# Performance work log

Hardware: AMD Instinct MI355X
Metric: run time of the kernel (lower is better)

Reference implementation:

```python
import math
import jax, jax.numpy as jnp
import numpy as np
from jax import lax

W_DIM = 512
UP = 2
K = 3
LRELU_GAIN = math.sqrt(2.0)  # bias_act def_gain for 'lrelu'
CLAMP = 256.0                # conv_clamp * gain(=1)


def setup_inputs() -> dict:
    key = jax.random.key(0)
    ks = jax.random.split(key, 8)
    B, Cin, Cout, H = 16, 512, 512, 32
    return {
        "x": jax.random.normal(ks[0], (B, Cin, H, H), jnp.float32),
        "w_latent": jax.random.normal(ks[1], (B, W_DIM), jnp.float32),
        "affine_weight": jax.random.normal(ks[2], (Cin, W_DIM), jnp.float32),
        "affine_bias": jnp.ones((Cin,), jnp.float32),  # bias_init=1
        "conv_weight": jax.random.normal(ks[3], (Cout, Cin, K, K), jnp.float32),
        "noise": jax.random.normal(ks[4], (B, 1, 2 * H, 2 * H), jnp.float32),
        "noise_strength": jax.random.uniform(ks[5], (1,), jnp.float32),
        "bias": jax.random.normal(ks[6], (Cout,), jnp.float32),
    }


def reference(x, w_latent, affine_weight, affine_bias, conv_weight, noise, noise_strength, bias):
    B, Cin, H, W = x.shape
    Cout = conv_weight.shape[0]

    # EqualFullyConnectedLayer (linear act): style = w @ (W * 1/sqrt(in)).T + b
    style = w_latent @ (affine_weight * (1.0 / math.sqrt(W_DIM))).T + affine_bias  # [B, Cin]

    # Modulate + demodulate per-sample weights: [B, Cout, Cin, K, K]
    wmod = conv_weight[None] * style[:, None, :, None, None]
    dcoefs = lax.rsqrt(jnp.sum(wmod * wmod, axis=(2, 3, 4)) + 1e-8)  # [B, Cout]
    wmod = wmod * dcoefs[:, :, None, None, None]

    # Grouped transposed conv (stride=UP), batch-as-groups trick.
    # torch.conv_transpose2d(x, w.transpose, stride=UP) == dilated conv with
    # spatially-flipped modulated weight, lhs_dilation=UP, padding=K-1.
    w_eff = wmod.reshape(B * Cout, Cin, K, K)[:, :, ::-1, ::-1]
    x1 = x.reshape(1, B * Cin, H, W)
    y = lax.conv_general_dilated(
        x1, w_eff, window_strides=(1, 1),
        padding=[(K - 1, K - 1), (K - 1, K - 1)],
        lhs_dilation=(UP, UP), feature_group_count=B,
        dimension_numbers=("NCHW", "OIHW", "NCHW"))  # [1, B*Cout, 2H+1, 2W+1]

    # upfirdn2d: FIR low-pass (1,3,3,1) outer, normalized, gain=up^2, pad (1,1,1,1)
    f1 = jnp.array([1.0, 3.0, 3.0, 1.0], jnp.float32)
    f2 = jnp.outer(f1, f1)
    f2 = f2 / f2.sum() * (UP * UP)
    yc = y.reshape(B * Cout, 1, 2 * H + 1, 2 * W + 1)
    y = lax.conv_general_dilated(
        yc, f2[None, None], window_strides=(1, 1), padding=[(1, 1), (1, 1)],
        dimension_numbers=("NCHW", "OIHW", "NCHW"))
    y = y.reshape(B, Cout, 2 * H, 2 * W)

    # noise injection + fused bias + lrelu(gain=sqrt(2)) + clamp
    y = y + noise * noise_strength[0]
    y = y + bias[None, :, None, None]
    y = jax.nn.leaky_relu(y, negative_slope=0.2) * LRELU_GAIN
    return jnp.clip(y, -CLAMP, CLAMP)
```

## Files before the change

### kernel.cpp

```cpp
#include <hip/hip_runtime.h>
#include <hip/hip_bf16.h>


typedef unsigned short u16;
typedef unsigned int u32;
typedef u16 u16x8 __attribute__((ext_vector_type(8)));
typedef __bf16 bf16x8 __attribute__((ext_vector_type(8)));
typedef float f32x4 __attribute__((ext_vector_type(4)));

#define NB 16

__device__ __forceinline__ float bf2f(u16 v) {
  unsigned int u = ((unsigned int)v) << 16;
  float f;
  __builtin_memcpy(&f, &u, 4);
  return f;
}
__device__ __forceinline__ u16 f2bf(float f) {
  __hip_bfloat16 h = __float2bfloat16(f);
  u16 r;
  __builtin_memcpy(&r, &h, 2);
  return r;
}
__device__ __forceinline__ void async16(u16* lds, const u16* g) {
  __builtin_amdgcn_global_load_lds(
      (const __attribute__((address_space(1))) u32*)g,
      (__attribute__((address_space(3))) u32*)lds, 16, 0, 0);
}

__global__ __launch_bounds__(256) void k_style(const float* __restrict__ wl,
                                               const float* __restrict__ aw,
                                               const float* __restrict__ ab,
                                               float* __restrict__ style) {
  __shared__ float lw[512];
  const int b = blockIdx.y;
  const int c0 = blockIdx.x << 6;
  const int t = threadIdx.x;
  for (int k = t; k < 512; k += 256) lw[k] = wl[b * 512 + k];
  __syncthreads();
  const int w = t >> 6, l = t & 63;
  const float4 lv0 = *(const float4*)(lw + (l << 2));
  const float4 lv1 = *(const float4*)(lw + 256 + (l << 2));
  for (int r = w; r < 64; r += 4) {
    const int c = c0 + r;
    const float* row = aw + (size_t)c * 512 + (l << 2);
    const float4 a0 = *(const float4*)(row);
    const float4 a1 = *(const float4*)(row + 256);
    float acc = lv0.x * a0.x + lv0.y * a0.y + lv0.z * a0.z + lv0.w * a0.w +
                lv1.x * a1.x + lv1.y * a1.y + lv1.z * a1.z + lv1.w * a1.w;
#pragma unroll
    for (int off = 32; off; off >>= 1) acc += __shfl_down(acc, off, 64);
    if (l == 0) style[b * 512 + c] = acc * 0.04419417382415922f + ab[c];
  }
}

__global__ __launch_bounds__(256) void k_wprep(const float* __restrict__ cw,
                                               const float* __restrict__ style,
                                               float* __restrict__ dcoef,
                                               u16* __restrict__ W2) {
  __shared__ u16 lw[4608];
  __shared__ float wsq[512];
  const int o = blockIdx.x, t = threadIdx.x;
  const float* src = cw + (size_t)o * 4608;
  for (int v = t; v < 4608; v += 256) {
    unsigned c = (unsigned)v / 9u;
    unsigned kp = (unsigned)v % 9u;
    lw[kp * 512 + c] = f2bf(src[v]);
  }
  for (int c = t; c < 512; c += 256) {
    const float* p = src + (size_t)c * 9;
    float s = 0.f;
#pragma unroll
    for (int k = 0; k < 9; ++k) {
      float v = p[k];
      s += v * v;
    }
    wsq[c] = s;
  }
  __syncthreads();
  u16* dst = W2 + (size_t)o * 4608;
  for (int v = t; v < 576; v += 256)
    *(u16x8*)(dst + v * 8) = *(const u16x8*)(lw + v * 8);
  const int w = t >> 6, l = t & 63;
  for (int b = w; b < NB; b += 4) {
    float part = 0.f;
#pragma unroll
    for (int c = l; c < 512; c += 64) {
      float st = style[b * 512 + c];
      part += st * st * wsq[c];
    }
#pragma unroll
    for (int off = 32; off; off >>= 1) part += __shfl_down(part, off, 64);
    if (l == 0) dcoef[b * 512 + o] = 1.0f / sqrtf(part + 1e-8f);
  }
}

__global__ __launch_bounds__(256) void k_xt(const float* __restrict__ x,
                                            const float* __restrict__ style,
                                            u16* __restrict__ xT) {
  __shared__ u16 tile[64 * 66];
  const int b = blockIdx.z, c0 = blockIdx.y << 6, s0 = blockIdx.x << 6;
  const int t = threadIdx.x;
#pragma unroll
  for (int i = 0; i < 16; ++i) {
    int e = i * 256 + t;
    int cc = e >> 6, ss = e & 63;
    int c = c0 + cc;
    float v = x[(size_t)(b * 512 + c) * 1024 + s0 + ss] * style[b * 512 + c];
    tile[cc * 66 + ss] = f2bf(v);
  }
  __syncthreads();
#pragma unroll
  for (int e = 0; e < 2; ++e) {
    int idx = e * 256 + t;
    int sc = idx >> 3;
    int cg = (idx & 7) << 3;
    u16x8 v;
#pragma unroll
    for (int g = 0; g < 8; ++g) v[g] = tile[(cg + g) * 66 + sc];
    *(u16x8*)(xT + (size_t)(b * 1024 + s0 + sc) * 512 + c0 + cg) = v;
  }
}

__global__ __launch_bounds__(512, 2) void k_gemm(const u16* __restrict__ W2,
                                                 const u16* __restrict__ xT,
                                                 u16* __restrict__ Z) {
  __shared__ u16 At[4][8192];
  __shared__ u16 Bt[4][8192];
  const int t = threadIdx.x;
  const int lin = blockIdx.y * 64 + blockIdx.x;
  const int xlog = ((lin & 7) << 3) | ((lin >> 3) & 7);
  const int ylog = lin >> 6;
  const int m0 = ylog << 8;
  const int n0 = xlog << 8;
  const int l = t & 63;
  const int w = t >> 6;
  const int wm = w >> 2;
  const int wn = w & 3;
  const int lrow = l & 15;
  const int lk = l >> 4;

  const int sr = t >> 2;
  const int sch = ((t & 3) + (sr >> 1)) & 3;
  const u16* gA = W2 + (size_t)(m0 + sr) * 512 + (sch << 3);
  const u16* gB = xT + (size_t)(n0 + sr) * 512 + (sch << 3);
  const int wb = w << 9;

  const int sk8 = ((lk - (lrow >> 1)) & 3) << 3;
  const int arow = (wm << 7) + lrow;
  const int brow = (wn << 6) + lrow;

  f32x4 acc[8][4] = {};

#define STAGE_A(nb_, kt_)                                   \
  async16(&At[nb_][wb], gA + (kt_) * 32);                   \
  async16(&At[nb_][4096 + wb], gA + (kt_) * 32 + 65536)
#define STAGE_B(nb_, kt_)                                   \
  async16(&Bt[nb_][wb], gB + (kt_) * 32);                   \
  async16(&Bt[nb_][4096 + wb], gB + (kt_) * 32 + 65536)

  STAGE_A(0, 0);
  STAGE_B(0, 0);
  STAGE_A(1, 1);
  STAGE_B(1, 1);
  STAGE_A(2, 2);
  STAGE_B(2, 2);
  asm volatile("s_waitcnt vmcnt(8)" ::: "memory");
  asm volatile("s_barrier" ::: "memory");

  for (int kt = 0; kt < 16; ++kt) {
    const int buf = kt & 3;
    const int nb = (kt + 3) & 3;
    const u16* Ab = At[buf];
    const u16* Bb = Bt[buf];
    bf16x8 av[4], bv[4], av2[4];

#pragma unroll
    for (int i = 0; i < 4; ++i)
      av[i] = *(const bf16x8*)(Ab + (arow + i * 16) * 32 + sk8);
#pragma unroll
    for (int j = 0; j < 4; ++j)
      bv[j] = *(const bf16x8*)(Bb + (brow + j * 16) * 32 + sk8);
    if (kt < 13) { STAGE_A(nb, kt + 3); }
    asm volatile("s_barrier" ::: "memory");
    asm volatile("s_waitcnt lgkmcnt(0)" ::: "memory");
    __builtin_amdgcn_sched_barrier(0);
    __builtin_amdgcn_s_setprio(1);
#pragma unroll
    for (int i = 0; i < 4; ++i)
#pragma unroll
      for (int j = 0; j < 4; ++j)
        acc[i][j] = __builtin_amdgcn_mfma_f32_16x16x32_bf16(av[i], bv[j], acc[i][j], 0, 0, 0);
    __builtin_amdgcn_s_setprio(0);
    asm volatile("s_barrier" ::: "memory");

#pragma unroll
    for (int i = 0; i < 4; ++i)
      av2[i] = *(const bf16x8*)(Ab + (arow + 64 + i * 16) * 32 + sk8);
    if (kt < 13) { STAGE_B(nb, kt + 3); }
    asm volatile("s_barrier" ::: "memory");
    asm volatile("s_waitcnt lgkmcnt(0)" ::: "memory");
    __builtin_amdgcn_sched_barrier(0);
    __builtin_amdgcn_s_setprio(1);
#pragma unroll
    for (int i = 0; i < 4; ++i)
#pragma unroll
      for (int j = 0; j < 4; ++j)
        acc[i + 4][j] = __builtin_amdgcn_mfma_f32_16x16x32_bf16(av2[i], bv[j], acc[i + 4][j], 0, 0, 0);
    __builtin_amdgcn_s_setprio(0);

    if (kt <= 12) {
      asm volatile("s_waitcnt vmcnt(8)" ::: "memory");
      asm volatile("s_barrier" ::: "memory");
    } else if (kt == 13) {
      asm volatile("s_waitcnt vmcnt(4)" ::: "memory");
      asm volatile("s_barrier" ::: "memory");
    } else if (kt == 14) {
      asm volatile("s_waitcnt vmcnt(0)" ::: "memory");
      asm volatile("s_barrier" ::: "memory");
    }
  }
#undef STAGE_A
#undef STAGE_B

  const int mr = m0 + (wm << 7) + (lk << 2);
  const int nc = n0 + (wn << 6) + lrow;
#pragma unroll
  for (int i = 0; i < 8; ++i)
#pragma unroll
    for (int j = 0; j < 4; ++j)
#pragma unroll
      for (int r = 0; r < 4; ++r)
        Z[(size_t)(mr + i * 16 + r) * 16384 + nc + j * 16] = f2bf(acc[i][j][r]);
}

__global__ __launch_bounds__(256) void k_scatter(
    const u16* __restrict__ Z, const float* __restrict__ dcoef,
    const float* __restrict__ noise, const float* __restrict__ nstr,
    const float* __restrict__ bias, float* __restrict__ out) {
  __shared__ u16 Zl[9 * 1024];
  __shared__ float Hl[3 * 2048];
  const int o = blockIdx.x;
  const int b = blockIdx.y;
  const int t = threadIdx.x;
  const u16* Zp = Z + (size_t)o * 9 * 16384 + (size_t)b * 1024;
  for (int v = t; v < 1152; v += 256) {
    int kp = v >> 7, off = (v & 127) << 3;
    *(u16x8*)(Zl + kp * 1024 + off) = *(const u16x8*)(Zp + (size_t)kp * 16384 + off);
  }
  __syncthreads();
#pragma unroll
  for (int e = 0; e < 12; ++e) {
    int idx = e * 256 + t;
    int ky = idx >> 10;
    int i = (idx >> 5) & 31;
    int j = idx & 31;
    const u16* P0 = Zl + (ky * 3 + 0) * 1024 + i * 32;
    const u16* P1 = P0 + 1024;
    const u16* P2 = P0 + 2048;
    float Ej = bf2f(P0[j]) + (j >= 1 ? bf2f(P2[j - 1]) : 0.f);
    float Ej1 = (j < 31 ? bf2f(P0[j + 1]) : 0.f) + bf2f(P2[j]);
    float Ojm = j >= 1 ? bf2f(P1[j - 1]) : 0.f;
    float Oj = bf2f(P1[j]);
    float Ojp = j < 31 ? bf2f(P1[j + 1]) : 0.f;
    float* hp = Hl + ky * 2048 + i * 64 + j;
    hp[0] = Ojm + 3.f * Ej + 3.f * Oj + Ej1;
    hp[32] = Ej + 3.f * Oj + 3.f * Ej1 + Ojp;
  }
  __syncthreads();
  const float dc = dcoef[b * 512 + o] * 0.0625f;
  const float ns = nstr[0];
  const float bo = bias[o];
  const int n = t & 63;
  const int i0 = (t >> 6) << 3;
  const int sw = ((n & 1) << 5) | (n >> 1);
  const float* H0 = Hl + sw;
  const float* H1 = Hl + 2048 + sw;
  const float* H2 = Hl + 4096 + sw;
  float h0 = H0[i0 * 64];
  float h1 = H1[i0 * 64];
  float h1p = (i0 > 0) ? H1[(i0 - 1) * 64] : 0.f;
  float h2p = (i0 > 0) ? H2[(i0 - 1) * 64] : 0.f;
  const float* nz = noise + ((size_t)b << 12) + n;
  float* op = out + (((size_t)(b * 512 + o)) << 12) + n;
#pragma unroll
  for (int s = 0; s < 8; ++s) {
    int i = i0 + s;
    float h0n = (i < 31) ? H0[(i + 1) * 64] : 0.f;
    float h1n = (i < 31) ? H1[(i + 1) * 64] : 0.f;
    float h2 = H2[i * 64];
    float ev = h1p + 3.f * (h0 + h2p) + 3.f * h1 + (h0n + h2);
    float od = (h0 + h2p) + 3.f * h1 + 3.f * (h0n + h2) + h1n;
    int m = 2 * i;
    float v0 = ev * dc + nz[(size_t)m * 64] * ns + bo;
    v0 = (v0 > 0.f ? v0 : 0.2f * v0) * 1.4142135623730951f;
    v0 = fminf(fmaxf(v0, -256.f), 256.f);
    op[(size_t)m * 64] = v0;
    float v1 = od * dc + nz[(size_t)(m + 1) * 64] * ns + bo;
    v1 = (v1 > 0.f ? v1 : 0.2f * v1) * 1.4142135623730951f;
    v1 = fminf(fmaxf(v1, -256.f), 256.f);
    op[(size_t)(m + 1) * 64] = v1;
    h0 = h0n;
    h1p = h1;
    h1 = h1n;
    h2p = h2;
  }
}

extern "C" void kernel_launch(void* const* d_in, const int* in_sizes, int n_in,
                              void* d_out, int out_size, void* d_ws, size_t ws_size,
                              hipStream_t stream) {
  const float* x = (const float*)d_in[0];
  const float* wl = (const float*)d_in[1];
  const float* aw = (const float*)d_in[2];
  const float* ab = (const float*)d_in[3];
  const float* cw = (const float*)d_in[4];
  const float* noise = (const float*)d_in[5];
  const float* nstr = (const float*)d_in[6];
  const float* bias = (const float*)d_in[7];
  float* out = (float*)d_out;

  float* style = (float*)d_ws;
  float* dcoef = style + 8192;
  u16* W2 = (u16*)(dcoef + 8192);
  u16* xT = W2 + 4608 * 512;
  u16* Z = xT + (size_t)16384 * 512;

  k_style<<<dim3(8, 16), 256, 0, stream>>>(wl, aw, ab, style);
  k_wprep<<<dim3(512), 256, 0, stream>>>(cw, style, dcoef, W2);
  k_xt<<<dim3(16, 8, 16), 256, 0, stream>>>(x, style, xT);
  k_gemm<<<dim3(64, 18), 512, 0, stream>>>(W2, xT, Z);
  k_scatter<<<dim3(512, 16), 256, 0, stream>>>(Z, dcoef, noise, nstr, bias, out);
}
```

Measured before the change: 392.8 us.

## Stage GEMM epilogue through LDS for coalesced stores; merge MFMA phases

New measurement: 379.3 us. 1.04x faster.

```diff
diff --git a/kernel.cpp b/kernel.cpp
--- a/kernel.cpp
+++ b/kernel.cpp
@@ -125,14 +125,13 @@
 __global__ __launch_bounds__(512, 2) void k_gemm(const u16* __restrict__ W2,
                                                  const u16* __restrict__ xT,
                                                  u16* __restrict__ Z) {
-  __shared__ u16 At[4][8192];
-  __shared__ u16 Bt[4][8192];
+  __shared__ union SM {
+    struct { u16 A[4][8192]; u16 B[4][8192]; } g;
+    u16 C[256 * 264];
+  } sm;
   const int t = threadIdx.x;
-  const int lin = blockIdx.y * 64 + blockIdx.x;
-  const int xlog = ((lin & 7) << 3) | ((lin >> 3) & 7);
-  const int ylog = lin >> 6;
-  const int m0 = ylog << 8;
-  const int n0 = xlog << 8;
+  const int m0 = blockIdx.y << 8;
+  const int n0 = blockIdx.x << 8;
   const int l = t & 63;
   const int w = t >> 6;
   const int wm = w >> 2;
@@ -153,11 +152,11 @@
   f32x4 acc[8][4] = {};
 
 #define STAGE_A(nb_, kt_)                                   \
-  async16(&At[nb_][wb], gA + (kt_) * 32);                   \
-  async16(&At[nb_][4096 + wb], gA + (kt_) * 32 + 65536)
+  async16(&sm.g.A[nb_][wb], gA + (kt_) * 32);               \
+  async16(&sm.g.A[nb_][4096 + wb], gA + (kt_) * 32 + 65536)
 #define STAGE_B(nb_, kt_)                                   \
-  async16(&Bt[nb_][wb], gB + (kt_) * 32);                   \
-  async16(&Bt[nb_][4096 + wb], gB + (kt_) * 32 + 65536)
+  async16(&sm.g.B[nb_][wb], gB + (kt_) * 32);               \
+  async16(&sm.g.B[nb_][4096 + wb], gB + (kt_) * 32 + 65536)
 
   STAGE_A(0, 0);
   STAGE_B(0, 0);
@@ -171,18 +170,22 @@
   for (int kt = 0; kt < 16; ++kt) {
     const int buf = kt & 3;
     const int nb = (kt + 3) & 3;
-    const u16* Ab = At[buf];
-    const u16* Bb = Bt[buf];
-    bf16x8 av[4], bv[4], av2[4];
-
+    const u16* Ab = sm.g.A[buf];
+    const u16* Bb = sm.g.B[buf];
+    bf16x8 av[4], av2[4], bv[4];
 #pragma unroll
     for (int i = 0; i < 4; ++i)
       av[i] = *(const bf16x8*)(Ab + (arow + i * 16) * 32 + sk8);
 #pragma unroll
+    for (int i = 0; i < 4; ++i)
+      av2[i] = *(const bf16x8*)(Ab + (arow + 64 + i * 16) * 32 + sk8);
+#pragma unroll
     for (int j = 0; j < 4; ++j)
       bv[j] = *(const bf16x8*)(Bb + (brow + j * 16) * 32 + sk8);
-    if (kt < 13) { STAGE_A(nb, kt + 3); }
-    asm volatile("s_barrier" ::: "memory");
+    if (kt < 13) {
+      STAGE_A(nb, kt + 3);
+      STAGE_B(nb, kt + 3);
+    }
     asm volatile("s_waitcnt lgkmcnt(0)" ::: "memory");
     __builtin_amdgcn_sched_barrier(0);
     __builtin_amdgcn_s_setprio(1);
@@ -191,24 +194,12 @@
 #pragma unroll
       for (int j = 0; j < 4; ++j)
         acc[i][j] = __builtin_amdgcn_mfma_f32_16x16x32_bf16(av[i], bv[j], acc[i][j], 0, 0, 0);
-    __builtin_amdgcn_s_setprio(0);
-    asm volatile("s_barrier" ::: "memory");
-
-#pragma unroll
-    for (int i = 0; i < 4; ++i)
-      av2[i] = *(const bf16x8*)(Ab + (arow + 64 + i * 16) * 32 + sk8);
-    if (kt < 13) { STAGE_B(nb, kt + 3); }
-    asm volatile("s_barrier" ::: "memory");
-    asm volatile("s_waitcnt lgkmcnt(0)" ::: "memory");
-    __builtin_amdgcn_sched_barrier(0);
-    __builtin_amdgcn_s_setprio(1);
 #pragma unroll
     for (int i = 0; i < 4; ++i)
 #pragma unroll
       for (int j = 0; j < 4; ++j)
         acc[i + 4][j] = __builtin_amdgcn_mfma_f32_16x16x32_bf16(av2[i], bv[j], acc[i + 4][j], 0, 0, 0);
     __builtin_amdgcn_s_setprio(0);
-
     if (kt <= 12) {
       asm volatile("s_waitcnt vmcnt(8)" ::: "memory");
       asm volatile("s_barrier" ::: "memory");
@@ -223,15 +214,25 @@
 #undef STAGE_A
 #undef STAGE_B
 
-  const int mr = m0 + (wm << 7) + (lk << 2);
-  const int nc = n0 + (wn << 6) + lrow;
+  __syncthreads();
+  const int crow0 = (wm << 7) + (lk << 2);
+  const int ccol0 = (wn << 6) + lrow;
 #pragma unroll
   for (int i = 0; i < 8; ++i)
 #pragma unroll
     for (int j = 0; j < 4; ++j)
 #pragma unroll
       for (int r = 0; r < 4; ++r)
-        Z[(size_t)(mr + i * 16 + r) * 16384 + nc + j * 16] = f2bf(acc[i][j][r]);
+        sm.C[(crow0 + i * 16 + r) * 264 + ccol0 + j * 16] = f2bf(acc[i][j][r]);
+  __syncthreads();
+  u16* zb = Z + (size_t)m0 * 16384 + n0;
+#pragma unroll
+  for (int k = 0; k < 16; ++k) {
+    int c = (k << 9) | t;
+    int row = c >> 5;
+    int c8 = (c & 31) << 3;
+    *(u16x8*)(zb + (size_t)row * 16384 + c8) = *(const u16x8*)(sm.C + row * 264 + c8);
+  }
 }
 
 __global__ __launch_bounds__(256) void k_scatter(
```
